# Optimization experiments

Measured on AMD Instinct MI355X. Metric: run time of the kernel, lower is better.

## Reference

```python
import jax, jax.numpy as jnp
import numpy as np


def setup_inputs() -> dict:
    key = jax.random.key(0)
    k_u, k_lam, k_B, k_C = jax.random.split(key, 4)
    batch, seq_len, d_model, N = 4, 4096, 1024, 64
    return {
        "u": jax.random.normal(k_u, (batch, seq_len, d_model), dtype=jnp.float32),
        "Lambda": jax.random.normal(k_lam, (N,), dtype=jnp.float32),
        "log_dt": jnp.zeros((1,), dtype=jnp.float32),
        "B": jax.random.normal(k_B, (N, d_model), dtype=jnp.float32),
        "C": jax.random.normal(k_C, (d_model, N), dtype=jnp.float32),
        "D": jnp.zeros((d_model,), dtype=jnp.float32),
    }


def reference(u, Lambda, log_dt, B, C, D):
    # dt = exp(log_dt); A = diag(exp(dt * (-exp(Lambda)))) -> diagonal decay vector a of shape (N,)
    dt = jnp.exp(log_dt)          # (1,)
    a = jnp.exp(-dt * jnp.exp(Lambda))  # (N,)

    # Precompute input projection for all timesteps: Bu[b, t, n] = u[b, t] @ B.T
    Bu = jnp.einsum("bld,nd->bln", u, B)  # (batch, L, N)

    # Sequential diagonal recurrence: x_t = a * x_{t-1} + Bu_t
    def step(x, bu_t):
        x = a * x + bu_t
        return x, x

    x0 = jnp.zeros((u.shape[0], Lambda.shape[0]), dtype=u.dtype)
    _, xs = jax.lax.scan(step, x0, jnp.swapaxes(Bu, 0, 1))  # xs: (L, batch, N)
    xs = jnp.swapaxes(xs, 0, 1)  # (batch, L, N)

    # Output projection + skip: y_t = x_t @ C.T + D * u_t
    return jnp.einsum("bln,dn->bld", xs, C) + D * u
```

## Files before the change

### kernel.cpp

```cpp
#include <hip/hip_runtime.h>
#include <hip/hip_bf16.h>


constexpr int BATCH  = 4;
constexpr int L      = 4096;
constexpr int DM     = 1024;
constexpr int N      = 64;
constexpr int ROWS   = BATCH * L;
constexpr int CHUNK  = 64;
constexpr int NCHUNK = L / CHUNK;

typedef __attribute__((ext_vector_type(8))) short     bf16x8;
typedef __attribute__((ext_vector_type(4))) float     f32x4;

__device__ __forceinline__ unsigned int pk2(float x, float y) {
  __hip_bfloat162 h = __float22bfloat162_rn(make_float2(x, y));
  return *reinterpret_cast<unsigned int*>(&h);
}

__global__ __launch_bounds__(256) void bu_scan(const float* __restrict__ u,
                                               const float* __restrict__ Bm,
                                               const float* __restrict__ Lambda,
                                               const float* __restrict__ log_dt,
                                               unsigned short* __restrict__ xsb,
                                               float* __restrict__ F) {
  __shared__ __align__(16) char smem[36864];
  typedef unsigned short HalfT[64][72];
  HalfT* As = reinterpret_cast<HalfT*>(smem);
  HalfT* Bs = reinterpret_cast<HalfT*>(smem + 18432);
  float (*T)[68] = reinterpret_cast<float (*)[68]>(smem);
  float* W = reinterpret_cast<float*>(smem + 17408);

  const int tid  = threadIdx.x;
  const int lane = tid & 63;
  const int wv   = tid >> 6;
  const int l15  = lane & 15;
  const int g    = lane >> 4;
  const int row0 = blockIdx.x * 64;

  const int sr = tid >> 4;
  const int sq = tid & 15;

  f32x4 acc[4] = {};
  float4 pa[2][4], pb[2][4];

  constexpr int NCH = DM / 64;
  #pragma unroll
  for (int s = 0; s < 2; ++s) {
    const int kb = s * 64;
    #pragma unroll
    for (int i = 0; i < 4; ++i) {
      const int r = sr + i * 16;
      pa[s][i] = *reinterpret_cast<const float4*>(&u[(long)(row0 + r) * DM + kb + sq * 4]);
      pb[s][i] = *reinterpret_cast<const float4*>(&Bm[(long)r * DM + kb + sq * 4]);
    }
  }

  #pragma unroll
  for (int c = 0; c < NCH; ++c) {
    const int s = c & 1;
    if (c) __syncthreads();
    #pragma unroll
    for (int i = 0; i < 4; ++i) {
      const int r = sr + i * 16;
      uint2 ha = {pk2(pa[s][i].x, pa[s][i].y), pk2(pa[s][i].z, pa[s][i].w)};
      uint2 hb = {pk2(pb[s][i].x, pb[s][i].y), pk2(pb[s][i].z, pb[s][i].w)};
      *reinterpret_cast<uint2*>(&As[s][r][sq * 4]) = ha;
      *reinterpret_cast<uint2*>(&Bs[s][r][sq * 4]) = hb;
    }
    __syncthreads();
    if (c + 2 < NCH) {
      const int kb = (c + 2) * 64;
      #pragma unroll
      for (int i = 0; i < 4; ++i) {
        const int r = sr + i * 16;
        pa[s][i] = *reinterpret_cast<const float4*>(&u[(long)(row0 + r) * DM + kb + sq * 4]);
        pb[s][i] = *reinterpret_cast<const float4*>(&Bm[(long)r * DM + kb + sq * 4]);
      }
    }
    #pragma unroll
    for (int ks = 0; ks < 2; ++ks) {
      const bf16x8 af = *reinterpret_cast<const bf16x8*>(
          &As[s][wv * 16 + l15][ks * 32 + g * 8]);
      #pragma unroll
      for (int t = 0; t < 4; ++t) {
        const bf16x8 bfr = *reinterpret_cast<const bf16x8*>(
            &Bs[s][t * 16 + l15][ks * 32 + g * 8]);
        acc[t] = __builtin_amdgcn_mfma_f32_16x16x32_bf16(af, bfr, acc[t], 0, 0, 0);
      }
    }
  }

  __syncthreads();
  #pragma unroll
  for (int t = 0; t < 4; ++t)
    #pragma unroll
    for (int r = 0; r < 4; ++r)
      T[wv * 16 + g * 4 + r][t * 16 + l15] = acc[t][r];
  __syncthreads();

  const float dtv = __expf(log_dt[0]);
  const float wn  = -dtv * __expf(Lambda[lane]);
  const float a   = __expf(wn);
  const float a16 = __expf(wn * 16.0f);

  float p[16];
  {
    float x = 0.0f;
    #pragma unroll
    for (int j = 0; j < 16; ++j) { x = fmaf(a, x, T[wv * 16 + j][lane]); p[j] = x; }
    W[wv * 64 + lane] = x;
  }
  __syncthreads();
  float P = 0.0f;
  #pragma unroll
  for (int w2 = 0; w2 < 3; ++w2)
    if (w2 < wv) P = fmaf(a16, P, W[w2 * 64 + lane]);
  __syncthreads();
  float cfac = P;
  #pragma unroll
  for (int j = 0; j < 16; ++j) { cfac *= a; T[wv * 16 + j][lane] = p[j] + cfac; }
  if (wv == 3) F[blockIdx.x * N + lane] = p[15] + cfac;
  __syncthreads();

  #pragma unroll
  for (int i = 0; i < 4; ++i) {
    const int idx = tid + i * 256;
    const int r = idx >> 4, q = idx & 15;
    const float4 v = *reinterpret_cast<const float4*>(&T[r][q * 4]);
    uint2 o = {pk2(v.x, v.y), pk2(v.z, v.w)};
    *reinterpret_cast<uint2*>(&xsb[(long)(row0 + r) * N + q * 4]) = o;
  }
}

__global__ __launch_bounds__(256) void carry_scan(const float* __restrict__ F,
                                                  const float* __restrict__ Lambda,
                                                  const float* __restrict__ log_dt,
                                                  float* __restrict__ carry,
                                                  float* __restrict__ dec) {
  const int t = threadIdx.x;
  const int b = t >> 6;
  const int n = t & 63;
  const float dt = __expf(log_dt[0]);
  const float w  = -dt * __expf(Lambda[n]);
  const float aS = __expf(w * (float)CHUNK);

  #pragma unroll
  for (int i = 0; i < 16; ++i) {
    const int tt = b * 16 + i;
    dec[tt * N + n] = __expf(w * (float)(tt + 1));
  }

  float f[NCHUNK];
  #pragma unroll
  for (int c = 0; c < NCHUNK; ++c) f[c] = F[(b * NCHUNK + c) * N + n];

  float P = 0.0f;
  #pragma unroll
  for (int c = 0; c < NCHUNK; ++c) {
    carry[(b * NCHUNK + c) * N + n] = P;
    P = fmaf(aS, P, f[c]);
  }
}

__global__ __launch_bounds__(256) void y_gemm(const unsigned short* __restrict__ xsb,
                                              const float* __restrict__ carry,
                                              const float* __restrict__ dec,
                                              const float* __restrict__ Cm,
                                              const float* __restrict__ Dv,
                                              const float* __restrict__ u,
                                              float* __restrict__ y) {
  __shared__ __align__(16) char smem[33792];
  unsigned short (*Xs)[72] = reinterpret_cast<unsigned short (*)[72]>(smem);
  unsigned short (*Cs)[72] = reinterpret_cast<unsigned short (*)[72]>(smem + 9216);
  float (*T)[132] = reinterpret_cast<float (*)[132]>(smem);
  __shared__ float ciS[64], Dsh[128];

  const int tid  = threadIdx.x;
  const int lane = tid & 63;
  const int wv   = tid >> 6;
  const int l15  = lane & 15;
  const int g    = lane >> 4;
  const int row0 = (blockIdx.x & 255) * 64;
  const int d0   = (blockIdx.x >> 8) * 128;

  if (tid < 64)  ciS[tid] = carry[row0 + tid];
  if (tid < 128) Dsh[tid] = Dv[d0 + tid];
  __syncthreads();

  #pragma unroll
  for (int i = 0; i < 2; ++i) {
    const int idx = tid + i * 256;
    const int r = idx >> 3, q = idx & 7;
    const uint4 xv = *reinterpret_cast<const uint4*>(&xsb[(long)(row0 + r) * N + q * 8]);
    const float4 dv0 = *reinterpret_cast<const float4*>(&dec[r * N + q * 8]);
    const float4 dv1 = *reinterpret_cast<const float4*>(&dec[r * N + q * 8 + 4]);
    float f[8];
    #pragma unroll
    for (int j = 0; j < 4; ++j) {
      const unsigned int wbits = (&xv.x)[j];
      f[2 * j]     = __uint_as_float(wbits << 16);
      f[2 * j + 1] = __uint_as_float(wbits & 0xFFFF0000u);
    }
    f[0] = fmaf(dv0.x, ciS[q * 8 + 0], f[0]);
    f[1] = fmaf(dv0.y, ciS[q * 8 + 1], f[1]);
    f[2] = fmaf(dv0.z, ciS[q * 8 + 2], f[2]);
    f[3] = fmaf(dv0.w, ciS[q * 8 + 3], f[3]);
    f[4] = fmaf(dv1.x, ciS[q * 8 + 4], f[4]);
    f[5] = fmaf(dv1.y, ciS[q * 8 + 5], f[5]);
    f[6] = fmaf(dv1.z, ciS[q * 8 + 6], f[6]);
    f[7] = fmaf(dv1.w, ciS[q * 8 + 7], f[7]);
    uint4 o = {pk2(f[0], f[1]), pk2(f[2], f[3]), pk2(f[4], f[5]), pk2(f[6], f[7])};
    *reinterpret_cast<uint4*>(&Xs[r][q * 8]) = o;
  }
  #pragma unroll
  for (int i = 0; i < 8; ++i) {
    const int idx = tid + i * 256;
    const int r = idx >> 4, q = idx & 15;
    const float4 v = *reinterpret_cast<const float4*>(&Cm[(long)(d0 + r) * N + q * 4]);
    uint2 o = {pk2(v.x, v.y), pk2(v.z, v.w)};
    *reinterpret_cast<uint2*>(&Cs[r][q * 4]) = o;
  }
  __syncthreads();

  bf16x8 af[2];
  #pragma unroll
  for (int ks = 0; ks < 2; ++ks)
    af[ks] = *reinterpret_cast<const bf16x8*>(&Xs[wv * 16 + l15][ks * 32 + g * 8]);

  f32x4 acc[8] = {};
  #pragma unroll
  for (int t = 0; t < 8; ++t) {
    #pragma unroll
    for (int ks = 0; ks < 2; ++ks) {
      const bf16x8 bfr = *reinterpret_cast<const bf16x8*>(
          &Cs[t * 16 + l15][ks * 32 + g * 8]);
      acc[t] = __builtin_amdgcn_mfma_f32_16x16x32_bf16(af[ks], bfr, acc[t], 0, 0, 0);
    }
  }

  __syncthreads();
  #pragma unroll
  for (int t = 0; t < 8; ++t)
    #pragma unroll
    for (int r = 0; r < 4; ++r)
      T[wv * 16 + g * 4 + r][t * 16 + l15] = acc[t][r];
  __syncthreads();

  #pragma unroll
  for (int i = 0; i < 8; ++i) {
    const int id = tid + i * 256;
    const int r = id >> 5;
    const int q = id & 31;
    float4 v = *reinterpret_cast<const float4*>(&T[r][q * 4]);
    const float4 dd = *reinterpret_cast<const float4*>(&Dsh[q * 4]);
    if (dd.x != 0.0f || dd.y != 0.0f || dd.z != 0.0f || dd.w != 0.0f) {
      const float4 uu = *reinterpret_cast<const float4*>(
          &u[(long)(row0 + r) * DM + d0 + q * 4]);
      v.x = fmaf(dd.x, uu.x, v.x);
      v.y = fmaf(dd.y, uu.y, v.y);
      v.z = fmaf(dd.z, uu.z, v.z);
      v.w = fmaf(dd.w, uu.w, v.w);
    }
    *reinterpret_cast<float4*>(&y[(long)(row0 + r) * DM + d0 + q * 4]) = v;
  }
}

extern "C" void kernel_launch(void* const* d_in, const int* in_sizes, int n_in,
                              void* d_out, int out_size, void* d_ws, size_t ws_size,
                              hipStream_t stream) {
  const float* u      = (const float*)d_in[0];
  const float* Lambda = (const float*)d_in[1];
  const float* log_dt = (const float*)d_in[2];
  const float* Bm     = (const float*)d_in[3];
  const float* Cm     = (const float*)d_in[4];
  const float* Dv     = (const float*)d_in[5];
  float* y = (float*)d_out;

  const size_t planeB = (size_t)ROWS * N;
  unsigned short* xsb = (unsigned short*)d_ws;
  float* F     = (float*)(xsb + planeB);
  float* carry = F + (size_t)BATCH * NCHUNK * N;
  float* dec   = carry + (size_t)BATCH * NCHUNK * N;

  bu_scan<<<ROWS / 64, 256, 0, stream>>>(u, Bm, Lambda, log_dt, xsb, F);
  carry_scan<<<1, 256, 0, stream>>>(F, Lambda, log_dt, carry, dec);
  y_gemm<<<(ROWS / 64) * (DM / 128), 256, 0, stream>>>(xsb, carry, dec, Cm, Dv, u, y);
}
```

Baseline: 36.07 us.

## Fuse carry scan into output GEMM kernel, recompute decay factors inline

Removes the single-block carry_scan launch. Each y_gemm block now computes its own chunk carry with a serial pass over the preceding chunk finals (up to 63 FMAs per state), and computes decay powers with exp instead of loading a precomputed table. This saves one kernel launch and a serialized tiny kernel between the two big ones. The cost is redundant carry work across the 8 d-column blocks and all chunks, plus extra exp instructions per element.

Result: no change. 36.24 us (+0.5%).

```diff
diff --git a/kernel.cpp b/kernel.cpp
--- a/kernel.cpp
+++ b/kernel.cpp
@@ -133,39 +133,10 @@
   }
 }
 
-__global__ __launch_bounds__(256) void carry_scan(const float* __restrict__ F,
-                                                  const float* __restrict__ Lambda,
-                                                  const float* __restrict__ log_dt,
-                                                  float* __restrict__ carry,
-                                                  float* __restrict__ dec) {
-  const int t = threadIdx.x;
-  const int b = t >> 6;
-  const int n = t & 63;
-  const float dt = __expf(log_dt[0]);
-  const float w  = -dt * __expf(Lambda[n]);
-  const float aS = __expf(w * (float)CHUNK);
-
-  #pragma unroll
-  for (int i = 0; i < 16; ++i) {
-    const int tt = b * 16 + i;
-    dec[tt * N + n] = __expf(w * (float)(tt + 1));
-  }
-
-  float f[NCHUNK];
-  #pragma unroll
-  for (int c = 0; c < NCHUNK; ++c) f[c] = F[(b * NCHUNK + c) * N + n];
-
-  float P = 0.0f;
-  #pragma unroll
-  for (int c = 0; c < NCHUNK; ++c) {
-    carry[(b * NCHUNK + c) * N + n] = P;
-    P = fmaf(aS, P, f[c]);
-  }
-}
-
 __global__ __launch_bounds__(256) void y_gemm(const unsigned short* __restrict__ xsb,
-                                              const float* __restrict__ carry,
-                                              const float* __restrict__ dec,
+                                              const float* __restrict__ F,
+                                              const float* __restrict__ Lambda,
+                                              const float* __restrict__ log_dt,
                                               const float* __restrict__ Cm,
                                               const float* __restrict__ Dv,
                                               const float* __restrict__ u,
@@ -174,7 +145,7 @@
   unsigned short (*Xs)[72] = reinterpret_cast<unsigned short (*)[72]>(smem);
   unsigned short (*Cs)[72] = reinterpret_cast<unsigned short (*)[72]>(smem + 9216);
   float (*T)[132] = reinterpret_cast<float (*)[132]>(smem);
-  __shared__ float ciS[64], Dsh[128];
+  __shared__ float ciS[64], wS[64], Dsh[128];
 
   const int tid  = threadIdx.x;
   const int lane = tid & 63;
@@ -183,9 +154,29 @@
   const int g    = lane >> 4;
   const int row0 = (blockIdx.x & 255) * 64;
   const int d0   = (blockIdx.x >> 8) * 128;
-
-  if (tid < 64)  ciS[tid] = carry[row0 + tid];
-  if (tid < 128) Dsh[tid] = Dv[d0 + tid];
+  const int b    = row0 >> 12;
+  const int c    = (row0 >> 6) & 63;
+
+  if (tid < 64) {
+    const int n = tid;
+    const float dtv = __expf(log_dt[0]);
+    const float wn  = -dtv * __expf(Lambda[n]);
+    wS[n] = wn;
+    const float aS = __expf(wn * 64.0f);
+    float P = 0.0f;
+    int j = 0;
+    for (; j + 16 <= c; j += 16) {
+      float fj[16];
+      #pragma unroll
+      for (int k = 0; k < 16; ++k) fj[k] = F[((b << 6) + j + k) * N + n];
+      #pragma unroll
+      for (int k = 0; k < 16; ++k) P = fmaf(aS, P, fj[k]);
+    }
+    for (; j < c; ++j) P = fmaf(aS, P, F[((b << 6) + j) * N + n]);
+    ciS[n] = P;
+  } else if (tid < 192) {
+    Dsh[tid - 64] = Dv[d0 + (tid - 64)];
+  }
   __syncthreads();
 
   #pragma unroll
@@ -193,8 +184,7 @@
     const int idx = tid + i * 256;
     const int r = idx >> 3, q = idx & 7;
     const uint4 xv = *reinterpret_cast<const uint4*>(&xsb[(long)(row0 + r) * N + q * 8]);
-    const float4 dv0 = *reinterpret_cast<const float4*>(&dec[r * N + q * 8]);
-    const float4 dv1 = *reinterpret_cast<const float4*>(&dec[r * N + q * 8 + 4]);
+    const float rp1 = (float)(r + 1);
     float f[8];
     #pragma unroll
     for (int j = 0; j < 4; ++j) {
@@ -202,14 +192,11 @@
       f[2 * j]     = __uint_as_float(wbits << 16);
       f[2 * j + 1] = __uint_as_float(wbits & 0xFFFF0000u);
     }
-    f[0] = fmaf(dv0.x, ciS[q * 8 + 0], f[0]);
-    f[1] = fmaf(dv0.y, ciS[q * 8 + 1], f[1]);
-    f[2] = fmaf(dv0.z, ciS[q * 8 + 2], f[2]);
-    f[3] = fmaf(dv0.w, ciS[q * 8 + 3], f[3]);
-    f[4] = fmaf(dv1.x, ciS[q * 8 + 4], f[4]);
-    f[5] = fmaf(dv1.y, ciS[q * 8 + 5], f[5]);
-    f[6] = fmaf(dv1.z, ciS[q * 8 + 6], f[6]);
-    f[7] = fmaf(dv1.w, ciS[q * 8 + 7], f[7]);
+    #pragma unroll
+    for (int j = 0; j < 8; ++j) {
+      const int n = q * 8 + j;
+      f[j] = fmaf(__expf(wS[n] * rp1), ciS[n], f[j]);
+    }
     uint4 o = {pk2(f[0], f[1]), pk2(f[2], f[3]), pk2(f[4], f[5]), pk2(f[6], f[7])};
     *reinterpret_cast<uint4*>(&Xs[r][q * 8]) = o;
   }
@@ -279,11 +266,9 @@
 
   const size_t planeB = (size_t)ROWS * N;
   unsigned short* xsb = (unsigned short*)d_ws;
-  float* F     = (float*)(xsb + planeB);
-  float* carry = F + (size_t)BATCH * NCHUNK * N;
-  float* dec   = carry + (size_t)BATCH * NCHUNK * N;
+  float* F = (float*)(xsb + planeB);
 
   bu_scan<<<ROWS / 64, 256, 0, stream>>>(u, Bm, Lambda, log_dt, xsb, F);
-  carry_scan<<<1, 256, 0, stream>>>(F, Lambda, log_dt, carry, dec);
-  y_gemm<<<(ROWS / 64) * (DM / 128), 256, 0, stream>>>(xsb, carry, dec, Cm, Dv, u, y);
-}
+  y_gemm<<<(ROWS / 64) * (DM / 128), 256, 0, stream>>>(xsb, F, Lambda, log_dt,
+                                                       Cm, Dv, u, y);
+}
```
